# Optimization experiments

Measured on AMD Instinct MI355X. Metric: run time of the kernel, lower is better.

The kernel has to match this reference:

```python
import jax, jax.numpy as jnp
import numpy as np

N = 100000      # total nodes across the batch of graphs
E = 1600000     # directed edges
G = 2048        # number of graphs (segments for mean pool)
DIN, DH, DOUT = 26, 128, 128


def setup_inputs() -> dict:
    key = jax.random.key(0)
    ks = jax.random.split(key, 10)
    x = jax.random.normal(ks[0], (N, DIN), dtype=jnp.float32)
    edge_index = jax.random.randint(ks[1], (2, E), 0, N, dtype=jnp.int64)
    batch = jnp.sort(jax.random.randint(ks[2], (N,), 0, G, dtype=jnp.int64))
    s = 0.1
    W1 = jax.random.normal(ks[3], (DIN, DH), jnp.float32) * s
    b1 = jnp.zeros((DH,), jnp.float32)
    W2 = jax.random.normal(ks[4], (DH, DH), jnp.float32) * s
    b2 = jnp.zeros((DH,), jnp.float32)
    W3 = jax.random.normal(ks[5], (DH, DOUT), jnp.float32) * s
    b3 = jnp.zeros((DOUT,), jnp.float32)
    return dict(x=x, edge_index=edge_index, batch=batch,
                W1=W1, b1=b1, W2=W2, b2=b2, W3=W3, b3=b3)


def reference(x, edge_index, batch, W1, b1, W2, b2, W3, b3):
    # GCNConv (PyG semantics): add self-loops, symmetric deg^-1/2 normalization,
    # linear transform, gather-scale-scatter aggregation, bias.
    loop = jnp.arange(N, dtype=edge_index.dtype)
    src = jnp.concatenate([edge_index[0], loop])
    dst = jnp.concatenate([edge_index[1], loop])
    deg = jax.ops.segment_sum(jnp.ones(src.shape, jnp.float32), dst, num_segments=N)
    dinv = jnp.where(deg > 0, jax.lax.rsqrt(deg), 0.0)
    norm = (dinv[src] * dinv[dst])[:, None]  # [E+N, 1]

    def gcn_conv(h, W, b):
        h = h @ W                                   # [N, d_out]
        msg = h[src] * norm                         # gather + scale (irregular)
        return jax.ops.segment_sum(msg, dst, num_segments=N) + b

    h = jax.nn.relu(gcn_conv(x, W1, b1))
    # F.dropout(p=0.1, training=self.training) -> identity in eval mode
    h = jax.nn.relu(gcn_conv(h, W2, b2))
    h = gcn_conv(h, W3, b3)

    # global_mean_pool over per-node graph ids
    sums = jax.ops.segment_sum(h, batch, num_segments=G)
    counts = jax.ops.segment_sum(jnp.ones((N, 1), jnp.float32), batch, num_segments=G)
    return sums / jnp.maximum(counts, 1.0)
```

## Files before the change

### kernel.cpp

```cpp
#include <hip/hip_runtime.h>
#include <hip/hip_bf16.h>


typedef __attribute__((ext_vector_type(8))) __bf16 bf16x8;
typedef __attribute__((ext_vector_type(4))) float f32x4;

union BF8 { bf16x8 v; unsigned short u[8]; };

#define BKT_SHIFT 9
#define BKT_NODES 512
#define EPB 8192

__device__ inline unsigned short f2bf(float f) {
    union { float f; unsigned u; } x; x.f = f;
    unsigned r = (x.u + 0x7FFFu + ((x.u >> 16) & 1u)) >> 16;
    return (unsigned short)r;
}
__device__ inline float bf2f(unsigned short u) {
    union { float f; unsigned u; } x; x.u = ((unsigned)u) << 16;
    return x.f;
}
__device__ inline float2 ld2bf(const unsigned short* p, size_t pair_idx) {
    unsigned v = ((const unsigned*)p)[pair_idx];
    union { float f; unsigned u; } a, b;
    a.u = (v & 0xFFFFu) << 16;
    b.u = v & 0xFFFF0000u;
    return make_float2(a.f, b.f);
}


__global__ __launch_bounds__(256) void bucket_hist_kernel(const int* __restrict__ dst,
                                                          int* __restrict__ bcount, int E) {
    __shared__ int lh[256];
    int t = threadIdx.x;
    lh[t] = 0;
    __syncthreads();
    int base = blockIdx.x * EPB;
    for (int i = t; i < EPB; i += 256) {
        int e = base + i;
        if (e < E) atomicAdd(&lh[dst[e] >> BKT_SHIFT], 1);
    }
    __syncthreads();
    if (lh[t]) atomicAdd(&bcount[t], lh[t]);
}

__global__ __launch_bounds__(256) void scan_buckets_kernel(const int* __restrict__ bcount,
                                                           int* __restrict__ blockoff,
                                                           int* __restrict__ bucket_cur, int NB) {
    __shared__ int sd[256];
    int t = threadIdx.x;
    int v = (t < NB) ? bcount[t] : 0;
    sd[t] = v;
    __syncthreads();
#pragma unroll
    for (int o = 1; o < 256; o <<= 1) {
        int u = (t >= o) ? sd[t - o] : 0;
        __syncthreads();
        sd[t] += u;
        __syncthreads();
    }
    if (t < NB) { int ex = sd[t] - v; blockoff[t] = ex; bucket_cur[t] = ex; }
    if (t == 255) blockoff[NB] = sd[255];
}

__global__ __launch_bounds__(256) void bucket_scatter_kernel(const int* __restrict__ src,
                                                             const int* __restrict__ dst,
                                                             int* __restrict__ bucket_cur,
                                                             int* __restrict__ ebuf, int E) {
    __shared__ int lh[256];
    __shared__ int lb[256];
    int t = threadIdx.x;
    lh[t] = 0;
    __syncthreads();
    int base = blockIdx.x * EPB;
    for (int i = t; i < EPB; i += 256) {
        int e = base + i;
        if (e < E) atomicAdd(&lh[dst[e] >> BKT_SHIFT], 1);
    }
    __syncthreads();
    int n = lh[t];
    if (n) lb[t] = atomicAdd(&bucket_cur[t], n);
    lh[t] = 0;
    __syncthreads();
    for (int i = t; i < EPB; i += 256) {
        int e = base + i;
        if (e < E) {
            int d = dst[e];
            int k = d >> BKT_SHIFT;
            int r = atomicAdd(&lh[k], 1);
            ebuf[lb[k] + r] = src[e] | ((d & (BKT_NODES - 1)) << 20);
        }
    }
}

__global__ __launch_bounds__(256) void bucket_csr_kernel(const int* __restrict__ ebuf,
                                                         const int* __restrict__ blockoff,
                                                         int* __restrict__ rowptr,
                                                         float* __restrict__ dinv,
                                                         int* __restrict__ csr, int N, int NB) {
    __shared__ int cnt[BKT_NODES];
    __shared__ int sd[256];
    int b = blockIdx.x, t = threadIdx.x;
    int node0 = b * BKT_NODES;
    int nn = min(BKT_NODES, N - node0);
    int ebase = blockoff[b];
    int ecnt = blockoff[b + 1] - ebase;
    cnt[t] = 0; cnt[t + 256] = 0;
    __syncthreads();
    for (int i = t; i < ecnt; i += 256)
        atomicAdd(&cnt[ebuf[ebase + i] >> 20], 1);
    __syncthreads();
    int c0 = cnt[2 * t], c1 = cnt[2 * t + 1];
    sd[t] = c0 + c1;
    __syncthreads();
#pragma unroll
    for (int o = 1; o < 256; o <<= 1) {
        int u = (t >= o) ? sd[t - o] : 0;
        __syncthreads();
        sd[t] += u;
        __syncthreads();
    }
    int ex = sd[t] - c0 - c1;
    if (2 * t < nn) {
        rowptr[node0 + 2 * t] = ebase + ex;
        dinv[node0 + 2 * t]   = rsqrtf((float)c0 + 1.0f);
    }
    if (2 * t + 1 < nn) {
        rowptr[node0 + 2 * t + 1] = ebase + ex + c0;
        dinv[node0 + 2 * t + 1]   = rsqrtf((float)c1 + 1.0f);
    }
    if (b == NB - 1 && t == 0) rowptr[N] = ebase + ecnt;
    __syncthreads();
    cnt[2 * t] = ex;
    cnt[2 * t + 1] = ex + c0;
    __syncthreads();
    for (int i = t; i < ecnt; i += 256) {
        int rec = ebuf[ebase + i];
        int p = atomicAdd(&cnt[rec >> 20], 1);
        csr[ebase + p] = rec & 0xFFFFF;
    }
}


__global__ __launch_bounds__(256) void wsplit_kernel(const float* __restrict__ W2,
                                                     const float* __restrict__ W3,
                                                     unsigned short* __restrict__ WT) {
    int t = blockIdx.x * blockDim.x + threadIdx.x;
    int which = t >> 14;
    int idx = t & 16383;
    int k = idx >> 7, c = idx & 127;
    const float* W = which ? W3 : W2;
    float w = W[k * 128 + c];
    unsigned short hi = f2bf(w);
    unsigned short lo = f2bf(w - bf2f(hi));
    unsigned short* Th = WT + (size_t)which * 2 * 16384;
    unsigned short* Tl = Th + 16384;
    Th[c * 128 + k] = hi;
    Tl[c * 128 + k] = lo;
}

__global__ __launch_bounds__(256) void wsplit1_kernel(const float* __restrict__ W1,
                                                      unsigned short* __restrict__ W1T) {
    int t = blockIdx.x * blockDim.x + threadIdx.x;
    int c = t >> 5, k = t & 31;
    float w = (k < 26) ? W1[k * 128 + c] : 0.f;
    unsigned short hi = f2bf(w);
    unsigned short lo = f2bf(w - bf2f(hi));
    W1T[c * 32 + k]        = hi;
    W1T[4096 + c * 32 + k] = lo;
}


__global__ __launch_bounds__(256) void aggx_kernel(const float* __restrict__ x,
                                                   const float* __restrict__ dinv,
                                                   const int* __restrict__ rowptr,
                                                   const int* __restrict__ csr,
                                                   float* __restrict__ y, int N) {
    int wid  = (int)((blockIdx.x * blockDim.x + threadIdx.x) >> 6);
    int lane = threadIdx.x & 63;
    if (wid >= N) return;
    const int i = wid;
    int start = __builtin_amdgcn_readfirstlane(rowptr[i]);
    int end   = __builtin_amdgcn_readfirstlane(rowptr[i + 1]);
    float di = dinv[i];
    float xv = (lane < 26) ? x[(size_t)i * 26 + lane] : 0.f;
    float acc = di * xv;
    int e = start;
    for (; e + 8 <= end; e += 8) {
        int idx[8];
#pragma unroll
        for (int j = 0; j < 8; ++j) idx[j] = csr[e + j];
#pragma unroll
        for (int j = 0; j < 8; ++j) {
            float v = (lane < 26) ? x[(size_t)idx[j] * 26 + lane] : 0.f;
            acc = fmaf(dinv[idx[j]], v, acc);
        }
    }
    for (; e < end; ++e) {
        int sn = csr[e];
        float v = (lane < 26) ? x[(size_t)sn * 26 + lane] : 0.f;
        acc = fmaf(dinv[sn], v, acc);
    }
    if (lane < 26) y[(size_t)i * 26 + lane] = acc * di;
}


__global__ __launch_bounds__(256) void mm1_mfma_kernel(const float* __restrict__ y,
                                                       const unsigned short* __restrict__ W1T,
                                                       const float* __restrict__ b1,
                                                       float* __restrict__ h, int N) {
    int wave = threadIdx.x >> 6;
    int lane = threadIdx.x & 63;
    int r0 = blockIdx.x * 64 + wave * 16;
    int arow = r0 + (lane & 15);
    int acl = min(arow, N - 1);
    int kgrp = lane >> 4;
    const float* yrow = y + (size_t)acl * 26;

    BF8 ah, al;
#pragma unroll
    for (int j = 0; j < 8; ++j) {
        int k = kgrp * 8 + j;
        float v = (k < 26) ? yrow[k] : 0.f;
        unsigned short hb = f2bf(v);
        ah.u[j] = hb;
        al.u[j] = f2bf(v - bf2f(hb));
    }

    const unsigned short* bh_base = W1T + (size_t)(lane & 15) * 32 + kgrp * 8;
    const unsigned short* bl_base = bh_base + 4096;

    f32x4 acc[8];
#pragma unroll
    for (int i = 0; i < 8; ++i) acc[i] = f32x4{0.f, 0.f, 0.f, 0.f};

#pragma unroll
    for (int ct = 0; ct < 8; ++ct) {
        BF8 bh, bl;
        bh.v = *(const bf16x8*)(bh_base + (size_t)ct * 16 * 32);
        bl.v = *(const bf16x8*)(bl_base + (size_t)ct * 16 * 32);
        acc[ct] = __builtin_amdgcn_mfma_f32_16x16x32_bf16(ah.v, bh.v, acc[ct], 0, 0, 0);
        acc[ct] = __builtin_amdgcn_mfma_f32_16x16x32_bf16(al.v, bh.v, acc[ct], 0, 0, 0);
        acc[ct] = __builtin_amdgcn_mfma_f32_16x16x32_bf16(ah.v, bl.v, acc[ct], 0, 0, 0);
    }

    int rbase = r0 + (lane >> 4) * 4;
#pragma unroll
    for (int r = 0; r < 4; ++r) {
        int row = rbase + r;
        if (row < N) {
#pragma unroll
            for (int ct = 0; ct < 8; ++ct) {
                int col = ct * 16 + (lane & 15);
                h[(size_t)row * 128 + col] = fmaxf(acc[ct][r] + b1[col], 0.f);
            }
        }
    }
}


__global__ __launch_bounds__(256) void mm_mfma_kernel(const float* __restrict__ h,
                                                      const unsigned short* __restrict__ WTh,
                                                      const unsigned short* __restrict__ WTl,
                                                      const float* __restrict__ dinv,
                                                      unsigned short* __restrict__ s, int N) {
    int wave = threadIdx.x >> 6;
    int lane = threadIdx.x & 63;
    int r0 = blockIdx.x * 64 + wave * 16;
    int arow = r0 + (lane & 15);
    int acl = min(arow, N - 1);
    int kgrp = lane >> 4;
    const float* hrow = h + (size_t)acl * 128 + kgrp * 8;

    f32x4 acc[8];
#pragma unroll
    for (int i = 0; i < 8; ++i) acc[i] = f32x4{0.f, 0.f, 0.f, 0.f};

    const unsigned short* bh_base = WTh + (size_t)(lane & 15) * 128 + kgrp * 8;
    const unsigned short* bl_base = WTl + (size_t)(lane & 15) * 128 + kgrp * 8;

#pragma unroll
    for (int ks = 0; ks < 4; ++ks) {
        const float4* p = (const float4*)(hrow + ks * 32);
        float4 v0 = p[0], v1 = p[1];
        float va[8] = {v0.x, v0.y, v0.z, v0.w, v1.x, v1.y, v1.z, v1.w};
        BF8 ah, al;
#pragma unroll
        for (int j = 0; j < 8; ++j) {
            unsigned short hb = f2bf(va[j]);
            ah.u[j] = hb;
            al.u[j] = f2bf(va[j] - bf2f(hb));
        }
#pragma unroll
        for (int ct = 0; ct < 8; ++ct) {
            BF8 bh, bl;
            bh.v = *(const bf16x8*)(bh_base + ks * 32 + (size_t)ct * 16 * 128);
            bl.v = *(const bf16x8*)(bl_base + ks * 32 + (size_t)ct * 16 * 128);
            acc[ct] = __builtin_amdgcn_mfma_f32_16x16x32_bf16(ah.v, bh.v, acc[ct], 0, 0, 0);
            acc[ct] = __builtin_amdgcn_mfma_f32_16x16x32_bf16(al.v, bh.v, acc[ct], 0, 0, 0);
            acc[ct] = __builtin_amdgcn_mfma_f32_16x16x32_bf16(ah.v, bl.v, acc[ct], 0, 0, 0);
        }
    }

    int rbase = r0 + (lane >> 4) * 4;
#pragma unroll
    for (int r = 0; r < 4; ++r) {
        int row = rbase + r;
        if (row < N) {
            float di = dinv[row];
#pragma unroll
            for (int ct = 0; ct < 8; ++ct) {
                int col = ct * 16 + (lane & 15);
                s[(size_t)row * 128 + col] = f2bf(acc[ct][r] * di);
            }
        }
    }
}


template <int RELU>
__global__ __launch_bounds__(256) void aggregate_kernel(const unsigned short* __restrict__ s,
                                                        const float* __restrict__ dinv,
                                                        const int* __restrict__ rowptr,
                                                        const int* __restrict__ csr,
                                                        const float* __restrict__ bias,
                                                        float* __restrict__ hout, int N) {
    int wid  = (int)((blockIdx.x * blockDim.x + threadIdx.x) >> 6);
    int lane = threadIdx.x & 63;
    if (wid >= N) return;
    const int i = wid;
    int start = __builtin_amdgcn_readfirstlane(rowptr[i]);
    int end   = __builtin_amdgcn_readfirstlane(rowptr[i + 1]);
    float2 acc = ld2bf(s, (size_t)i * 64 + lane);
    int e = start;
    for (; e + 8 <= end; e += 8) {
        int idx[8];
#pragma unroll
        for (int j = 0; j < 8; ++j) idx[j] = csr[e + j];
#pragma unroll
        for (int j = 0; j < 8; ++j) {
            float2 v = ld2bf(s, (size_t)idx[j] * 64 + lane);
            acc.x += v.x; acc.y += v.y;
        }
    }
    for (; e < end; ++e) {
        int sn = csr[e];
        float2 v = ld2bf(s, (size_t)sn * 64 + lane);
        acc.x += v.x; acc.y += v.y;
    }
    float di = dinv[i];
    float2 bv = ((const float2*)bias)[lane];
    float ox = acc.x * di + bv.x;
    float oy = acc.y * di + bv.y;
    if (RELU) { ox = fmaxf(ox, 0.f); oy = fmaxf(oy, 0.f); }
    ((float2*)hout)[(size_t)i * 64 + lane] = make_float2(ox, oy);
}


__global__ __launch_bounds__(128) void pool_kernel(const float* __restrict__ h,
                                                   const int* __restrict__ batch,
                                                   float* __restrict__ out, int N) {
    int g = blockIdx.x;
    int j = threadIdx.x;
    int lo = 0, hi = N;
    while (lo < hi) { int mid = (lo + hi) >> 1; if (batch[mid] < g) lo = mid + 1; else hi = mid; }
    int start = lo;
    hi = N;
    while (lo < hi) { int mid = (lo + hi) >> 1; if (batch[mid] < g + 1) lo = mid + 1; else hi = mid; }
    int end = lo;
    float acc = 0.f;
    for (int i = start; i < end; ++i) acc += h[(size_t)i * 128 + j];
    int cnt = end - start;
    out[(size_t)g * 128 + j] = acc / (float)max(cnt, 1);
}


extern "C" void kernel_launch(void* const* d_in, const int* in_sizes, int n_in,
                              void* d_out, int out_size, void* d_ws, size_t ws_size,
                              hipStream_t stream) {
    const float* x     = (const float*)d_in[0];
    const int*   edge  = (const int*)d_in[1];
    const int*   batch = (const int*)d_in[2];
    const float* W1    = (const float*)d_in[3];
    const float* b1    = (const float*)d_in[4];
    const float* W2    = (const float*)d_in[5];
    const float* b2    = (const float*)d_in[6];
    const float* W3    = (const float*)d_in[7];
    const float* b3    = (const float*)d_in[8];
    float* out = (float*)d_out;

    const int N = in_sizes[2];
    const int E = in_sizes[1] / 2;
    const int G = out_size / 128;

    const int* src = edge;
    const int* dst = edge + E;

    char* base = (char*)d_ws;
    size_t off = 0;
    auto carve = [&](size_t bytes) -> char* {
        char* p = base + off;
        off = (off + bytes + 255) & ~(size_t)255;
        return p;
    };
    int*            rowptr     = (int*)carve((size_t)(N + 1) * 4);
    float*          dinv       = (float*)carve((size_t)N * 4);
    int*            csr        = (int*)carve((size_t)E * 4);
    int*            ebuf       = (int*)carve((size_t)E * 4);
    unsigned short* WT         = (unsigned short*)carve((size_t)4 * 16384 * 2);
    unsigned short* W1T        = (unsigned short*)carve((size_t)2 * 4096 * 2);
    int*            bcount     = (int*)carve(256 * 4);
    int*            blockoff   = (int*)carve(260 * 4);
    int*            bucket_cur = (int*)carve(256 * 4);
    float*          ybuf       = (float*)carve((size_t)N * 26 * 4);
    float*          bufH       = (float*)carve((size_t)N * 128 * 4);
    unsigned short* bufS       = (unsigned short*)carve((size_t)N * 128 * 2);

    if (off > ws_size) {
        hipMemsetAsync(d_out, 0, (size_t)out_size * 4, stream);
        return;
    }

    const int NB   = (N + BKT_NODES - 1) / BKT_NODES;
    const int EBK  = (E + EPB - 1) / EPB;

    hipMemsetAsync(bcount, 0, 256 * 4, stream);
    bucket_hist_kernel<<<EBK, 256, 0, stream>>>(dst, bcount, E);
    scan_buckets_kernel<<<1, 256, 0, stream>>>(bcount, blockoff, bucket_cur, NB);
    bucket_scatter_kernel<<<EBK, 256, 0, stream>>>(src, dst, bucket_cur, ebuf, E);
    bucket_csr_kernel<<<NB, 256, 0, stream>>>(ebuf, blockoff, rowptr, dinv, csr, N, NB);
    wsplit_kernel<<<128, 256, 0, stream>>>(W2, W3, WT);
    wsplit1_kernel<<<16, 256, 0, stream>>>(W1, W1T);

    const unsigned short* WT2h = WT;
    const unsigned short* WT2l = WT + 16384;
    const unsigned short* WT3h = WT + 2 * 16384;
    const unsigned short* WT3l = WT + 3 * 16384;

    int mfbk = (N + 63) / 64;
    int agbk = (N + 3) / 4;

    aggx_kernel<<<agbk, 256, 0, stream>>>(x, dinv, rowptr, csr, ybuf, N);
    mm1_mfma_kernel<<<mfbk, 256, 0, stream>>>(ybuf, W1T, b1, bufH, N);
    mm_mfma_kernel<<<mfbk, 256, 0, stream>>>(bufH, WT2h, WT2l, dinv, bufS, N);
    aggregate_kernel<1><<<agbk, 256, 0, stream>>>(bufS, dinv, rowptr, csr, b2, bufH, N);
    mm_mfma_kernel<<<mfbk, 256, 0, stream>>>(bufH, WT3h, WT3l, dinv, bufS, N);
    aggregate_kernel<0><<<agbk, 256, 0, stream>>>(bufS, dinv, rowptr, csr, b3, bufH, N);
    pool_kernel<<<G, 128, 0, stream>>>(bufH, batch, out, N);
}
```

Baseline: 507.1 us.

## Process multiple edges per wave with vectorized gathers in aggregation kernels

```diff
diff --git a/kernel.cpp b/kernel.cpp
--- a/kernel.cpp
+++ b/kernel.cpp
@@ -20,12 +20,11 @@
     union { float f; unsigned u; } x; x.u = ((unsigned)u) << 16;
     return x.f;
 }
-__device__ inline float2 ld2bf(const unsigned short* p, size_t pair_idx) {
-    unsigned v = ((const unsigned*)p)[pair_idx];
-    union { float f; unsigned u; } a, b;
-    a.u = (v & 0xFFFFu) << 16;
-    b.u = v & 0xFFFF0000u;
-    return make_float2(a.f, b.f);
+__device__ inline float bflo(unsigned v) {
+    union { float f; unsigned u; } x; x.u = (v & 0xFFFFu) << 16; return x.f;
+}
+__device__ inline float bfhi(unsigned v) {
+    union { float f; unsigned u; } x; x.u = v & 0xFFFF0000u; return x.f;
 }
 
 
@@ -171,41 +170,67 @@
 }
 
 
-__global__ __launch_bounds__(256) void aggx_kernel(const float* __restrict__ x,
-                                                   const float* __restrict__ dinv,
-                                                   const int* __restrict__ rowptr,
-                                                   const int* __restrict__ csr,
-                                                   float* __restrict__ y, int N) {
+__global__ __launch_bounds__(256) void xpad_kernel(const float* __restrict__ x,
+                                                   float* __restrict__ xp, int N) {
+    int t = blockIdx.x * blockDim.x + threadIdx.x;
+    if (t >= N * 32) return;
+    int i = t >> 5, k = t & 31;
+    xp[t] = (k < 26) ? x[(size_t)i * 26 + k] : 0.f;
+}
+
+
+__global__ __launch_bounds__(256) void aggx8_kernel(const float* __restrict__ xp,
+                                                    const float* __restrict__ dinv,
+                                                    const int* __restrict__ rowptr,
+                                                    const int* __restrict__ csr,
+                                                    float* __restrict__ yp, int N) {
     int wid  = (int)((blockIdx.x * blockDim.x + threadIdx.x) >> 6);
     int lane = threadIdx.x & 63;
     if (wid >= N) return;
     const int i = wid;
     int start = __builtin_amdgcn_readfirstlane(rowptr[i]);
     int end   = __builtin_amdgcn_readfirstlane(rowptr[i + 1]);
-    float di = dinv[i];
-    float xv = (lane < 26) ? x[(size_t)i * 26 + lane] : 0.f;
-    float acc = di * xv;
+    int grp = lane >> 3;
+    int fl  = lane & 7;
+
+    float4 acc = make_float4(0.f, 0.f, 0.f, 0.f);
     int e = start;
     for (; e + 8 <= end; e += 8) {
-        int idx[8];
-#pragma unroll
-        for (int j = 0; j < 8; ++j) idx[j] = csr[e + j];
-#pragma unroll
-        for (int j = 0; j < 8; ++j) {
-            float v = (lane < 26) ? x[(size_t)idx[j] * 26 + lane] : 0.f;
-            acc = fmaf(dinv[idx[j]], v, acc);
-        }
-    }
-    for (; e < end; ++e) {
-        int sn = csr[e];
-        float v = (lane < 26) ? x[(size_t)sn * 26 + lane] : 0.f;
-        acc = fmaf(dinv[sn], v, acc);
-    }
-    if (lane < 26) y[(size_t)i * 26 + lane] = acc * di;
-}
-
-
-__global__ __launch_bounds__(256) void mm1_mfma_kernel(const float* __restrict__ y,
+        int ci = csr[e + grp];
+        float dv = dinv[ci];
+        float4 v = *(const float4*)(xp + (size_t)ci * 32 + fl * 4);
+        acc.x = fmaf(dv, v.x, acc.x); acc.y = fmaf(dv, v.y, acc.y);
+        acc.z = fmaf(dv, v.z, acc.z); acc.w = fmaf(dv, v.w, acc.w);
+    }
+    if (e < end) {
+        int e0 = e + grp;
+        if (e0 < end) {
+            int ci = csr[e0];
+            float dv = dinv[ci];
+            float4 v = *(const float4*)(xp + (size_t)ci * 32 + fl * 4);
+            acc.x = fmaf(dv, v.x, acc.x); acc.y = fmaf(dv, v.y, acc.y);
+            acc.z = fmaf(dv, v.z, acc.z); acc.w = fmaf(dv, v.w, acc.w);
+        }
+    }
+#pragma unroll
+    for (int off = 8; off <= 32; off <<= 1) {
+        acc.x += __shfl_xor(acc.x, off);
+        acc.y += __shfl_xor(acc.y, off);
+        acc.z += __shfl_xor(acc.z, off);
+        acc.w += __shfl_xor(acc.w, off);
+    }
+    float di = dinv[i];
+    float4 xv = *(const float4*)(xp + (size_t)i * 32 + fl * 4);
+    acc.x = fmaf(di, xv.x, acc.x); acc.y = fmaf(di, xv.y, acc.y);
+    acc.z = fmaf(di, xv.z, acc.z); acc.w = fmaf(di, xv.w, acc.w);
+    if (grp == 0) {
+        float4 o = make_float4(acc.x * di, acc.y * di, acc.z * di, acc.w * di);
+        *(float4*)(yp + (size_t)i * 32 + fl * 4) = o;
+    }
+}
+
+
+__global__ __launch_bounds__(256) void mm1_mfma_kernel(const float* __restrict__ yp,
                                                        const unsigned short* __restrict__ W1T,
                                                        const float* __restrict__ b1,
                                                        float* __restrict__ h, int N) {
@@ -215,16 +240,17 @@
     int arow = r0 + (lane & 15);
     int acl = min(arow, N - 1);
     int kgrp = lane >> 4;
-    const float* yrow = y + (size_t)acl * 26;
-
+    const float* yrow = yp + (size_t)acl * 32 + kgrp * 8;
+
+    float4 v0 = ((const float4*)yrow)[0];
+    float4 v1 = ((const float4*)yrow)[1];
+    float va[8] = {v0.x, v0.y, v0.z, v0.w, v1.x, v1.y, v1.z, v1.w};
     BF8 ah, al;
 #pragma unroll
     for (int j = 0; j < 8; ++j) {
-        int k = kgrp * 8 + j;
-        float v = (k < 26) ? yrow[k] : 0.f;
-        unsigned short hb = f2bf(v);
+        unsigned short hb = f2bf(va[j]);
         ah.u[j] = hb;
-        al.u[j] = f2bf(v - bf2f(hb));
+        al.u[j] = f2bf(va[j] - bf2f(hb));
     }
 
     const unsigned short* bh_base = W1T + (size_t)(lane & 15) * 32 + kgrp * 8;
@@ -319,41 +345,79 @@
 
 
 template <int RELU>
-__global__ __launch_bounds__(256) void aggregate_kernel(const unsigned short* __restrict__ s,
-                                                        const float* __restrict__ dinv,
-                                                        const int* __restrict__ rowptr,
-                                                        const int* __restrict__ csr,
-                                                        const float* __restrict__ bias,
-                                                        float* __restrict__ hout, int N) {
+__global__ __launch_bounds__(256) void aggregate4_kernel(const unsigned short* __restrict__ s,
+                                                         const float* __restrict__ dinv,
+                                                         const int* __restrict__ rowptr,
+                                                         const int* __restrict__ csr,
+                                                         const float* __restrict__ bias,
+                                                         float* __restrict__ hout, int N) {
     int wid  = (int)((blockIdx.x * blockDim.x + threadIdx.x) >> 6);
     int lane = threadIdx.x & 63;
     if (wid >= N) return;
     const int i = wid;
     int start = __builtin_amdgcn_readfirstlane(rowptr[i]);
     int end   = __builtin_amdgcn_readfirstlane(rowptr[i + 1]);
-    float2 acc = ld2bf(s, (size_t)i * 64 + lane);
+    int grp = lane >> 4;
+    int fl  = lane & 15;
+
+    float acc[8];
+#pragma unroll
+    for (int j = 0; j < 8; ++j) acc[j] = 0.f;
+
     int e = start;
     for (; e + 8 <= end; e += 8) {
-        int idx[8];
-#pragma unroll
-        for (int j = 0; j < 8; ++j) idx[j] = csr[e + j];
-#pragma unroll
-        for (int j = 0; j < 8; ++j) {
-            float2 v = ld2bf(s, (size_t)idx[j] * 64 + lane);
-            acc.x += v.x; acc.y += v.y;
-        }
-    }
-    for (; e < end; ++e) {
-        int sn = csr[e];
-        float2 v = ld2bf(s, (size_t)sn * 64 + lane);
-        acc.x += v.x; acc.y += v.y;
+        int ci0 = csr[e + grp];
+        int ci1 = csr[e + 4 + grp];
+        uint4 w0 = *(const uint4*)(s + (size_t)ci0 * 128 + fl * 8);
+        uint4 w1 = *(const uint4*)(s + (size_t)ci1 * 128 + fl * 8);
+        acc[0] += bflo(w0.x); acc[1] += bfhi(w0.x);
+        acc[2] += bflo(w0.y); acc[3] += bfhi(w0.y);
+        acc[4] += bflo(w0.z); acc[5] += bfhi(w0.z);
+        acc[6] += bflo(w0.w); acc[7] += bfhi(w0.w);
+        acc[0] += bflo(w1.x); acc[1] += bfhi(w1.x);
+        acc[2] += bflo(w1.y); acc[3] += bfhi(w1.y);
+        acc[4] += bflo(w1.z); acc[5] += bfhi(w1.z);
+        acc[6] += bflo(w1.w); acc[7] += bfhi(w1.w);
+    }
+    if (e < end) {
+        int e0 = e + grp, e1 = e + 4 + grp;
+        if (e0 < end) {
+            int ci = csr[e0];
+            uint4 w = *(const uint4*)(s + (size_t)ci * 128 + fl * 8);
+            acc[0] += bflo(w.x); acc[1] += bfhi(w.x);
+            acc[2] += bflo(w.y); acc[3] += bfhi(w.y);
+            acc[4] += bflo(w.z); acc[5] += bfhi(w.z);
+            acc[6] += bflo(w.w); acc[7] += bfhi(w.w);
+        }
+        if (e1 < end) {
+            int ci = csr[e1];
+            uint4 w = *(const uint4*)(s + (size_t)ci * 128 + fl * 8);
+            acc[0] += bflo(w.x); acc[1] += bfhi(w.x);
+            acc[2] += bflo(w.y); acc[3] += bfhi(w.y);
+            acc[4] += bflo(w.z); acc[5] += bfhi(w.z);
+            acc[6] += bflo(w.w); acc[7] += bfhi(w.w);
+        }
+    }
+#pragma unroll
+    for (int off = 16; off <= 32; off <<= 1) {
+#pragma unroll
+        for (int j = 0; j < 8; ++j) acc[j] += __shfl_xor(acc[j], off);
+    }
+    {
+        uint4 w = *(const uint4*)(s + (size_t)i * 128 + fl * 8);
+        acc[0] += bflo(w.x); acc[1] += bfhi(w.x);
+        acc[2] += bflo(w.y); acc[3] += bfhi(w.y);
+        acc[4] += bflo(w.z); acc[5] += bfhi(w.z);
+        acc[6] += bflo(w.w); acc[7] += bfhi(w.w);
     }
     float di = dinv[i];
-    float2 bv = ((const float2*)bias)[lane];
-    float ox = acc.x * di + bv.x;
-    float oy = acc.y * di + bv.y;
+    int j0 = grp * 2;
+    int f = fl * 8 + j0;
+    const float2 bv = ((const float2*)bias)[f >> 1];
+    float ox = acc[j0] * di + bv.x;
+    float oy = acc[j0 + 1] * di + bv.y;
     if (RELU) { ox = fmaxf(ox, 0.f); oy = fmaxf(oy, 0.f); }
-    ((float2*)hout)[(size_t)i * 64 + lane] = make_float2(ox, oy);
+    ((float2*)hout)[(size_t)i * 64 + (f >> 1)] = make_float2(ox, oy);
 }
 
 
@@ -412,7 +476,8 @@
     int*            bcount     = (int*)carve(256 * 4);
     int*            blockoff   = (int*)carve(260 * 4);
     int*            bucket_cur = (int*)carve(256 * 4);
-    float*          ybuf       = (float*)carve((size_t)N * 26 * 4);
+    float*          xp         = (float*)carve((size_t)N * 32 * 4);
+    float*          yp         = (float*)carve((size_t)N * 32 * 4);
     float*          bufH       = (float*)carve((size_t)N * 128 * 4);
     unsigned short* bufS       = (unsigned short*)carve((size_t)N * 128 * 2);
 
@@ -431,6 +496,7 @@
     bucket_csr_kernel<<<NB, 256, 0, stream>>>(ebuf, blockoff, rowptr, dinv, csr, N, NB);
     wsplit_kernel<<<128, 256, 0, stream>>>(W2, W3, WT);
     wsplit1_kernel<<<16, 256, 0, stream>>>(W1, W1T);
+    xpad_kernel<<<(N * 32 + 255) / 256, 256, 0, stream>>>(x, xp, N);
 
     const unsigned short* WT2h = WT;
     const unsigned short* WT2l = WT + 16384;
@@ -440,11 +506,11 @@
     int mfbk = (N + 63) / 64;
     int agbk = (N + 3) / 4;
 
-    aggx_kernel<<<agbk, 256, 0, stream>>>(x, dinv, rowptr, csr, ybuf, N);
-    mm1_mfma_kernel<<<mfbk, 256, 0, stream>>>(ybuf, W1T, b1, bufH, N);
+    aggx8_kernel<<<agbk, 256, 0, stream>>>(xp, dinv, rowptr, csr, yp, N);
+    mm1_mfma_kernel<<<mfbk, 256, 0, stream>>>(yp, W1T, b1, bufH, N);
     mm_mfma_kernel<<<mfbk, 256, 0, stream>>>(bufH, WT2h, WT2l, dinv, bufS, N);
-    aggregate_kernel<1><<<agbk, 256, 0, stream>>>(bufS, dinv, rowptr, csr, b2, bufH, N);
+    aggregate4_kernel<1><<<agbk, 256, 0, stream>>>(bufS, dinv, rowptr, csr, b2, bufH, N);
     mm_mfma_kernel<<<mfbk, 256, 0, stream>>>(bufH, WT3h, WT3l, dinv, bufS, N);
-    aggregate_kernel<0><<<agbk, 256, 0, stream>>>(bufS, dinv, rowptr, csr, b3, bufH, N);
+    aggregate4_kernel<0><<<agbk, 256, 0, stream>>>(bufS, dinv, rowptr, csr, b3, bufH, N);
     pool_kernel<<<G, 128, 0, stream>>>(bufH, batch, out, N);
 }
```

Result: faster. 495.4 us (-2.3%).
